# Kernel tuning notes

Measured on AMD Instinct MI355X. Metric: run time of the kernel, lower is better.

The kernel has to match this reference:

```python
import jax, jax.numpy as jnp
import numpy as np


def pairwise_dist(x):
    # Euclidean cdist via the expansion trick; grad-safe sqrt (0 grad at 0, like torch).
    sq = jnp.sum(x * x, axis=1)
    d2 = sq[:, None] + sq[None, :] - 2.0 * (x @ x.T)
    d2 = jnp.maximum(d2, 0.0)
    pos = d2 > 0
    return jnp.where(pos, jnp.sqrt(jnp.where(pos, d2, 1.0)), 0.0)


def knn_mask(dist, k):
    # per-row ascending sort; skip index 0 (self), take next k neighbors
    idx = jnp.argsort(dist, axis=1)[:, 1:k + 1]            # [N, k]
    n = dist.shape[0]
    return jnp.zeros_like(dist).at[jnp.arange(n)[:, None], idx].set(1.0)


def setup_inputs() -> dict:
    key = jax.random.key(0)
    k1, k2 = jax.random.split(key)
    N, D, K = 8192, 64, 12
    latent = jax.random.normal(k1, (N, D), dtype=jnp.float32)
    latent_norm = jnp.ones((), dtype=jnp.float32)
    X = jax.random.normal(k2, (N, D), dtype=jnp.float32)
    dist_X = pairwise_dist(X)
    pair_mask_X = knn_mask(dist_X, K)
    return {"latent": latent, "latent_norm": latent_norm,
            "dist_X": dist_X, "pair_mask_X": pair_mask_X, "k": K}


def reference(latent, latent_norm, dist_X, pair_mask_X, k):
    n = latent.shape[0]
    dist_Z = pairwise_dist(latent) / latent_norm
    pair_mask_Z = knn_mask(dist_Z, k)

    mask_diff = pair_mask_Z - pair_mask_X
    matched = (n * k - jnp.sum(mask_diff != 0) * 0.5) / (n * k)

    # match_edges == 'symmetric'
    sig1 = dist_X * pair_mask_X
    sig1_2 = dist_Z * pair_mask_X
    distance1_2 = jnp.sum(jnp.square(sig1 - sig1_2))
    sig2 = dist_Z * pair_mask_Z
    sig2_1 = dist_X * pair_mask_Z
    distance2_1 = jnp.sum(jnp.square(sig2_1 - sig2))
    distance = distance1_2 + distance2_1
    return (distance, matched, distance1_2, distance2_1)
```

## Files before the change

### kernel.cpp

```cpp
#include <hip/hip_runtime.h>
#include <stdint.h>

constexpr int NPTS = 8192;
constexpr int DIM  = 64;
constexpr int KNN  = 12;

constexpr int RT = 64;
constexpr int CT = 64;
constexpr int CS = 4;
constexpr int STRIPE = NPTS / CS;
constexpr int NCHUNK = STRIPE / CT;
constexpr int LSTR = 72;
constexpr int BSTR = 65;

constexpr int NWG_DZ = (NPTS / RT) * CS;
constexpr int TOT4   = NPTS * NPTS / 4;
constexpr int WG4    = TOT4 / NWG_DZ;
constexpr int CH4    = WG4 / NCHUNK;

constexpr unsigned long long SENTINEL = 0xFFFFFFFFFFFFFFFFull;

typedef short bf16x8 __attribute__((ext_vector_type(8)));
typedef float f32x4  __attribute__((ext_vector_type(4)));

#define WG_BARRIER() asm volatile("s_waitcnt lgkmcnt(0)\n\ts_barrier" ::: "memory")

__device__ __forceinline__ unsigned short f2bf(float x) {
  unsigned u = __float_as_uint(x);
  return (unsigned short)((u + 0x7FFFu + ((u >> 16) & 1u)) >> 16);
}
__device__ __forceinline__ float bf2f(unsigned short h) {
  return __uint_as_float(((unsigned)h) << 16);
}

__global__ __launch_bounds__(256) void prep_kernel(
    const float* __restrict__ latent, unsigned short* __restrict__ Lh,
    unsigned short* __restrict__ Ll, float* __restrict__ sq,
    int* __restrict__ ecnt, float* __restrict__ out) {
  int i = blockIdx.x * 256 + threadIdx.x;
  ecnt[i] = 0;
  if (i < 4) out[i] = 0.0f;
  const float4* p = reinterpret_cast<const float4*>(latent + (size_t)i * DIM);
  float s = 0.f;
#pragma unroll
  for (int t = 0; t < DIM / 4; ++t) {
    float4 v = p[t];
    s += v.x * v.x + v.y * v.y + v.z * v.z + v.w * v.w;
    ushort4 h, l;
    h.x = f2bf(v.x); l.x = f2bf(v.x - bf2f(h.x));
    h.y = f2bf(v.y); l.y = f2bf(v.y - bf2f(h.y));
    h.z = f2bf(v.z); l.z = f2bf(v.z - bf2f(h.z));
    h.w = f2bf(v.w); l.w = f2bf(v.w - bf2f(h.w));
    *reinterpret_cast<ushort4*>(Lh + (size_t)i * DIM + t * 4) = h;
    *reinterpret_cast<ushort4*>(Ll + (size_t)i * DIM + t * 4) = l;
  }
  sq[i] = s;
}

__device__ __forceinline__ void topk_insert(unsigned long long cand,
                                            unsigned long long pk[KNN]) {
#pragma unroll
  for (int s = KNN - 1; s >= 0; --s) {
    bool belongs = cand < pk[s];
    bool shift = (s > 0) && (cand < pk[s - 1]);
    unsigned long long nv = shift ? pk[s - 1] : cand;
    if (belongs) pk[s] = nv;
  }
}

__device__ __forceinline__ void push_edge(int pos, int* __restrict__ ecnt,
                                          int* __restrict__ ecol) {
  int i = pos >> 13, j = pos & (NPTS - 1);
  int slot = atomicAdd(&ecnt[i], 1);
  if (slot < KNN) ecol[i * KNN + slot] = j;
}

__global__ __launch_bounds__(256, 2) void main_kernel(
    const unsigned short* __restrict__ Lh, const unsigned short* __restrict__ Ll,
    const float* __restrict__ sq, unsigned long long* __restrict__ topk_ws,
    const float* __restrict__ mask_X, int* __restrict__ ecnt,
    int* __restrict__ ecol) {
  __shared__ unsigned short Bh[CT * LSTR], Bl[CT * LSTR];
  __shared__ float d2b[RT * BSTR];
  __shared__ int   colb[RT * BSTR];
  __shared__ int   cnt[RT];
  __shared__ float thr[RT];
  __shared__ float sqA[RT];
  __shared__ float sqB[CT];

  const int tid = threadIdx.x;
  const int tile = blockIdx.x / CS;
  const int split = blockIdx.x % CS;
  const int ib = tile * RT;
  const int jb0 = split * STRIPE;

  const int wid = tid >> 6;
  const int lane = tid & 63;
  const int quad = lane >> 4;
  const int l16 = lane & 15;
  const int wr = wid >> 1;
  const int wc = wid & 1;

  bf16x8 ahr[2][2], alr[2][2];
#pragma unroll
  for (int kk = 0; kk < 2; ++kk) {
    const int ko = kk * 32 + quad * 8;
#pragma unroll
    for (int rb = 0; rb < 2; ++rb) {
      const int row = ib + wr * 32 + rb * 16 + l16;
      ahr[kk][rb] = *reinterpret_cast<const bf16x8*>(Lh + (size_t)row * DIM + ko);
      alr[kk][rb] = *reinterpret_cast<const bf16x8*>(Ll + (size_t)row * DIM + ko);
    }
  }
  if (tid < RT) { sqA[tid] = sq[ib + tid]; thr[tid] = 3.4e38f; }

  const f32x4* mbase = reinterpret_cast<const f32x4*>(mask_X);
  const int wgBase4 = blockIdx.x * WG4;

  unsigned long long pk[KNN];
#pragma unroll
  for (int t = 0; t < KNN; ++t) pk[t] = SENTINEL;

  for (int ch = 0; ch < NCHUNK; ++ch) {
    const int jb = jb0 + ch * CT;
    WG_BARRIER();

#pragma unroll
    for (int it = 0; it < 2; ++it) {
      int f = it * 256 + tid;
      int r = f >> 3, c = f & 7;
      uint4 vh = *reinterpret_cast<const uint4*>(Lh + (size_t)(jb + r) * DIM + c * 8);
      uint4 vl = *reinterpret_cast<const uint4*>(Ll + (size_t)(jb + r) * DIM + c * 8);
      *reinterpret_cast<uint4*>(&Bh[r * LSTR + c * 8]) = vh;
      *reinterpret_cast<uint4*>(&Bl[r * LSTR + c * 8]) = vl;
    }
    if (tid < CT) sqB[tid] = sq[jb + tid];
    if (tid < RT) cnt[tid] = 0;

    __builtin_amdgcn_sched_barrier(0);
    f32x4 m[4];
    const int mb = wgBase4 + ch * CH4 + tid;
#pragma unroll
    for (int q = 0; q < 4; ++q)
      m[q] = __builtin_nontemporal_load(&mbase[mb + q * 256]);

    WG_BARRIER();

    f32x4 acc[2][2];
#pragma unroll
    for (int rb = 0; rb < 2; ++rb)
#pragma unroll
      for (int cb = 0; cb < 2; ++cb) acc[rb][cb] = (f32x4){0.f, 0.f, 0.f, 0.f};

#pragma unroll
    for (int kk = 0; kk < 2; ++kk) {
      const int ko = kk * 32 + quad * 8;
      bf16x8 bh[2], bl[2];
#pragma unroll
      for (int cb = 0; cb < 2; ++cb) {
        int col = wc * 32 + cb * 16 + l16;
        bh[cb] = *reinterpret_cast<const bf16x8*>(&Bh[col * LSTR + ko]);
        bl[cb] = *reinterpret_cast<const bf16x8*>(&Bl[col * LSTR + ko]);
      }
#pragma unroll
      for (int rb = 0; rb < 2; ++rb)
#pragma unroll
        for (int cb = 0; cb < 2; ++cb) {
          acc[rb][cb] = __builtin_amdgcn_mfma_f32_16x16x32_bf16(ahr[kk][rb], bh[cb], acc[rb][cb], 0, 0, 0);
          acc[rb][cb] = __builtin_amdgcn_mfma_f32_16x16x32_bf16(ahr[kk][rb], bl[cb], acc[rb][cb], 0, 0, 0);
          acc[rb][cb] = __builtin_amdgcn_mfma_f32_16x16x32_bf16(alr[kk][rb], bh[cb], acc[rb][cb], 0, 0, 0);
        }
    }

#pragma unroll
    for (int rb = 0; rb < 2; ++rb) {
      const int row0 = wr * 32 + rb * 16 + quad * 4;
#pragma unroll
      for (int r = 0; r < 4; ++r) {
        const int rl = row0 + r;
        const int gi = ib + rl;
        const float sa = sqA[rl];
        const float t_thr = thr[rl];
#pragma unroll
        for (int cb = 0; cb < 2; ++cb) {
          const int col_l = wc * 32 + cb * 16 + l16;
          const int gj = jb + col_l;
          float d2 = sa + sqB[col_l] - 2.0f * acc[rb][cb][r];
          float d2c = fmaxf(d2, 0.0f);
          if (d2c < t_thr && gj != gi) {
            int pos = atomicAdd(&cnt[rl], 1);
            d2b[rl * BSTR + pos] = d2c;
            colb[rl * BSTR + pos] = gj;
          }
        }
      }
    }
    WG_BARRIER();

    if (tid < RT) {
      int n = cnt[tid];
      for (int t = 0; t < n; ++t) {
        unsigned long long cand =
            ((unsigned long long)__float_as_uint(d2b[tid * BSTR + t]) << 32) |
            (unsigned)colb[tid * BSTR + t];
        if (cand < pk[KNN - 1]) topk_insert(cand, pk);
      }
      thr[tid] = __uint_as_float((unsigned)(pk[KNN - 1] >> 32));
    }

#pragma unroll
    for (int q = 0; q < 4; ++q) {
      f32x4 mv = m[q];
      if (mv[0] == 0.f && mv[1] == 0.f && mv[2] == 0.f && mv[3] == 0.f) continue;
      const int base = (mb + q * 256) * 4;
      if (mv[0] != 0.f) push_edge(base + 0, ecnt, ecol);
      if (mv[1] != 0.f) push_edge(base + 1, ecnt, ecol);
      if (mv[2] != 0.f) push_edge(base + 2, ecnt, ecol);
      if (mv[3] != 0.f) push_edge(base + 3, ecnt, ecol);
    }
  }

  if (tid < RT) {
    size_t base = ((size_t)(ib + tid) * CS + split) * KNN;
#pragma unroll
    for (int t = 0; t < KNN; ++t) topk_ws[base + t] = pk[t];
  }
}

__global__ __launch_bounds__(256) void tail_kernel(
    const float* __restrict__ latent, const float* __restrict__ latent_norm,
    const float* __restrict__ dist_X, const int* __restrict__ ecol,
    const unsigned long long* __restrict__ topk_ws, float* __restrict__ d_out) {
  __shared__ float red[256];
  const int tid = threadIdx.x;
  const float invnorm = 1.0f / latent_norm[0];

  if (blockIdx.x < (NPTS * KNN / 256)) {
    const int e = blockIdx.x * 256 + tid;
    int i = e / KNN;
    int j = ecol[e];
    float dx = dist_X[(size_t)i * NPTS + j];
    const float4* a = reinterpret_cast<const float4*>(latent + (size_t)i * DIM);
    const float4* b = reinterpret_cast<const float4*>(latent + (size_t)j * DIM);
    float d2 = 0.f;
#pragma unroll
    for (int t = 0; t < DIM / 4; ++t) {
      float4 va = a[t], vb = b[t];
      float ex = va.x - vb.x, ey = va.y - vb.y, ez = va.z - vb.z, ew = va.w - vb.w;
      d2 += ex * ex + ey * ey + ez * ez + ew * ew;
    }
    float dz = (d2 > 0.f) ? sqrtf(d2) * invnorm : 0.f;
    float diff = dx - dz;

    red[tid] = diff * diff;
    __syncthreads();
    for (int s = 128; s > 0; s >>= 1) {
      if (tid < s) red[tid] += red[tid + s];
      __syncthreads();
    }
    if (tid == 0) {
      atomicAdd(&d_out[2], red[0]);
      atomicAdd(&d_out[0], red[0]);
    }
  } else {
    const int gi = (blockIdx.x - NPTS * KNN / 256) * 256 + tid;

    unsigned long long pk[KNN];
#pragma unroll
    for (int t = 0; t < KNN; ++t) pk[t] = SENTINEL;

    const unsigned long long* src = topk_ws + (size_t)gi * CS * KNN;
    for (int t = 0; t < CS * KNN; ++t) {
      unsigned long long cand = src[t];
      if (cand < pk[KNN - 1]) topk_insert(cand, pk);
    }

    int ec[KNN];
#pragma unroll
    for (int t = 0; t < KNN; ++t) ec[t] = ecol[gi * KNN + t];

    float acc2 = 0.f, accc = 0.f;
#pragma unroll
    for (int t = 0; t < KNN; ++t) {
      int j = (int)(unsigned)(pk[t] & 0xFFFFFFFFull);
      float d2 = __uint_as_float((unsigned)(pk[t] >> 32));
      float dz = (d2 > 0.0f) ? sqrtf(d2) * invnorm : 0.0f;
      float dxv = dist_X[(size_t)gi * NPTS + j];
      float diff = dxv - dz;
      acc2 += diff * diff;
      int hit = 0;
#pragma unroll
      for (int s = 0; s < KNN; ++s) hit |= (ec[s] == j);
      accc += (float)hit;
    }

    red[tid] = acc2;
    __syncthreads();
    for (int s = 128; s > 0; s >>= 1) {
      if (tid < s) red[tid] += red[tid + s];
      __syncthreads();
    }
    float racc2 = red[0];
    __syncthreads();
    red[tid] = accc;
    __syncthreads();
    for (int s = 128; s > 0; s >>= 1) {
      if (tid < s) red[tid] += red[tid + s];
      __syncthreads();
    }
    if (tid == 0) {
      atomicAdd(&d_out[3], racc2);
      atomicAdd(&d_out[0], racc2);
      atomicAdd(&d_out[1], red[0] * (1.0f / ((float)NPTS * (float)KNN)));
    }
  }
}

extern "C" void kernel_launch(void* const* d_in, const int* in_sizes, int n_in,
                              void* d_out, int out_size, void* d_ws,
                              size_t ws_size, hipStream_t stream) {
  const float* latent      = (const float*)d_in[0];
  const float* latent_norm = (const float*)d_in[1];
  const float* dist_X      = (const float*)d_in[2];
  const float* mask_X      = (const float*)d_in[3];
  float* out = (float*)d_out;

  char* w = (char*)d_ws;
  float*          sq   = (float*)w;                    w += NPTS * 4;
  unsigned short* Lh   = (unsigned short*)w;           w += NPTS * DIM * 2;
  unsigned short* Ll   = (unsigned short*)w;           w += NPTS * DIM * 2;
  int*            ecnt = (int*)w;                      w += NPTS * 4;
  int*            ecol = (int*)w;                      w += NPTS * KNN * 4;
  unsigned long long* topk = (unsigned long long*)w;

  prep_kernel<<<NPTS / 256, 256, 0, stream>>>(latent, Lh, Ll, sq, ecnt, out);
  main_kernel<<<NWG_DZ, 256, 0, stream>>>(Lh, Ll, sq, topk, mask_X, ecnt, ecol);
  tail_kernel<<<NPTS * KNN / 256 + NPTS / 256, 256, 0, stream>>>(
      latent, latent_norm, dist_X, ecol, topk, out);
}
```

Baseline: 620.7 us.

## Double-buffer column tiles, shrink candidate buffers with overflow retry, raise occupancy

Column tiles are now double-buffered: the next chunk's global loads are issued before the MFMA work and written to the alternate LDS buffer, which removes one barrier per chunk and hides load latency. The per-row candidate buffer shrinks from 65 to 28 entries, and an overflow loop reprocesses any leftover candidates, so LDS use drops. With less LDS per block and twice as many column splits, the occupancy hint rises from 2 to 3 workgroups and there are more, shorter workgroups. The cost is extra retry rounds when a row overflows, which is likely in early chunks while the threshold is still loose, plus the higher register pressure that the tighter launch bound brings.

After: 707.4 us. 14.0% more time.

```diff
diff --git a/kernel.cpp b/kernel.cpp
--- a/kernel.cpp
+++ b/kernel.cpp
@@ -7,11 +7,12 @@
 
 constexpr int RT = 64;
 constexpr int CT = 64;
-constexpr int CS = 4;
+constexpr int CS = 8;
 constexpr int STRIPE = NPTS / CS;
 constexpr int NCHUNK = STRIPE / CT;
 constexpr int LSTR = 72;
-constexpr int BSTR = 65;
+constexpr int CAP  = 28;
+constexpr int BSTR = 29;
 
 constexpr int NWG_DZ = (NPTS / RT) * CS;
 constexpr int TOT4   = NPTS * NPTS / 4;
@@ -75,18 +76,19 @@
   if (slot < KNN) ecol[i * KNN + slot] = j;
 }
 
-__global__ __launch_bounds__(256, 2) void main_kernel(
+__global__ __launch_bounds__(256, 3) void main_kernel(
     const unsigned short* __restrict__ Lh, const unsigned short* __restrict__ Ll,
     const float* __restrict__ sq, unsigned long long* __restrict__ topk_ws,
     const float* __restrict__ mask_X, int* __restrict__ ecnt,
     int* __restrict__ ecol) {
-  __shared__ unsigned short Bh[CT * LSTR], Bl[CT * LSTR];
+  __shared__ unsigned short Bh[2 * CT * LSTR], Bl[2 * CT * LSTR];
   __shared__ float d2b[RT * BSTR];
   __shared__ int   colb[RT * BSTR];
   __shared__ int   cnt[RT];
   __shared__ float thr[RT];
   __shared__ float sqA[RT];
-  __shared__ float sqB[CT];
+  __shared__ float sqB[2][CT];
+  __shared__ int   ovf;
 
   const int tid = threadIdx.x;
   const int tile = blockIdx.x / CS;
@@ -112,7 +114,20 @@
       alr[kk][rb] = *reinterpret_cast<const bf16x8*>(Ll + (size_t)row * DIM + ko);
     }
   }
-  if (tid < RT) { sqA[tid] = sq[ib + tid]; thr[tid] = 3.4e38f; }
+  if (tid < RT) { sqA[tid] = sq[ib + tid]; thr[tid] = 3.4e38f; cnt[tid] = 0; }
+
+  {
+#pragma unroll
+    for (int it = 0; it < 2; ++it) {
+      int f = it * 256 + tid, r = f >> 3, c = f & 7;
+      uint4 vh = *reinterpret_cast<const uint4*>(Lh + (size_t)(jb0 + r) * DIM + c * 8);
+      uint4 vl = *reinterpret_cast<const uint4*>(Ll + (size_t)(jb0 + r) * DIM + c * 8);
+      *reinterpret_cast<uint4*>(&Bh[r * LSTR + c * 8]) = vh;
+      *reinterpret_cast<uint4*>(&Bl[r * LSTR + c * 8]) = vl;
+    }
+    if (tid < CT) sqB[0][tid] = sq[jb0 + tid];
+  }
+  __syncthreads();
 
   const f32x4* mbase = reinterpret_cast<const f32x4*>(mask_X);
   const int wgBase4 = blockIdx.x * WG4;
@@ -122,30 +137,33 @@
   for (int t = 0; t < KNN; ++t) pk[t] = SENTINEL;
 
   for (int ch = 0; ch < NCHUNK; ++ch) {
+    const int cur = ch & 1, nxt = cur ^ 1;
     const int jb = jb0 + ch * CT;
-    WG_BARRIER();
-
-#pragma unroll
-    for (int it = 0; it < 2; ++it) {
-      int f = it * 256 + tid;
-      int r = f >> 3, c = f & 7;
-      uint4 vh = *reinterpret_cast<const uint4*>(Lh + (size_t)(jb + r) * DIM + c * 8);
-      uint4 vl = *reinterpret_cast<const uint4*>(Ll + (size_t)(jb + r) * DIM + c * 8);
-      *reinterpret_cast<uint4*>(&Bh[r * LSTR + c * 8]) = vh;
-      *reinterpret_cast<uint4*>(&Bl[r * LSTR + c * 8]) = vl;
-    }
-    if (tid < CT) sqB[tid] = sq[jb + tid];
-    if (tid < RT) cnt[tid] = 0;
-
-    __builtin_amdgcn_sched_barrier(0);
+    const bool have_next = (ch + 1 < NCHUNK);
+
+    uint4 vh0, vl0, vh1, vl1;
+    float sqn = 0.f;
+    if (have_next) {
+      {
+        int f = tid, r = f >> 3, c = f & 7;
+        vh0 = *reinterpret_cast<const uint4*>(Lh + (size_t)(jb + CT + r) * DIM + c * 8);
+        vl0 = *reinterpret_cast<const uint4*>(Ll + (size_t)(jb + CT + r) * DIM + c * 8);
+      }
+      {
+        int f = 256 + tid, r = f >> 3, c = f & 7;
+        vh1 = *reinterpret_cast<const uint4*>(Lh + (size_t)(jb + CT + r) * DIM + c * 8);
+        vl1 = *reinterpret_cast<const uint4*>(Ll + (size_t)(jb + CT + r) * DIM + c * 8);
+      }
+      if (tid < CT) sqn = sq[jb + CT + tid];
+    }
     f32x4 m[4];
     const int mb = wgBase4 + ch * CH4 + tid;
 #pragma unroll
     for (int q = 0; q < 4; ++q)
       m[q] = __builtin_nontemporal_load(&mbase[mb + q * 256]);
-
-    WG_BARRIER();
-
+    __builtin_amdgcn_sched_barrier(0);
+
+    const int bbase = cur * CT * LSTR;
     f32x4 acc[2][2];
 #pragma unroll
     for (int rb = 0; rb < 2; ++rb)
@@ -159,8 +177,8 @@
 #pragma unroll
       for (int cb = 0; cb < 2; ++cb) {
         int col = wc * 32 + cb * 16 + l16;
-        bh[cb] = *reinterpret_cast<const bf16x8*>(&Bh[col * LSTR + ko]);
-        bl[cb] = *reinterpret_cast<const bf16x8*>(&Bl[col * LSTR + ko]);
+        bh[cb] = *reinterpret_cast<const bf16x8*>(&Bh[bbase + col * LSTR + ko]);
+        bl[cb] = *reinterpret_cast<const bf16x8*>(&Bl[bbase + col * LSTR + ko]);
       }
 #pragma unroll
       for (int rb = 0; rb < 2; ++rb)
@@ -172,52 +190,81 @@
         }
     }
 
-#pragma unroll
-    for (int rb = 0; rb < 2; ++rb) {
-      const int row0 = wr * 32 + rb * 16 + quad * 4;
-#pragma unroll
-      for (int r = 0; r < 4; ++r) {
-        const int rl = row0 + r;
-        const int gi = ib + rl;
-        const float sa = sqA[rl];
-        const float t_thr = thr[rl];
-#pragma unroll
-        for (int cb = 0; cb < 2; ++cb) {
-          const int col_l = wc * 32 + cb * 16 + l16;
-          const int gj = jb + col_l;
-          float d2 = sa + sqB[col_l] - 2.0f * acc[rb][cb][r];
-          float d2c = fmaxf(d2, 0.0f);
-          if (d2c < t_thr && gj != gi) {
-            int pos = atomicAdd(&cnt[rl], 1);
-            d2b[rl * BSTR + pos] = d2c;
-            colb[rl * BSTR + pos] = gj;
+    unsigned todo = 0xFFFFu;
+    int round = 0;
+    do {
+#pragma unroll
+      for (int rb = 0; rb < 2; ++rb) {
+#pragma unroll
+        for (int r = 0; r < 4; ++r) {
+          const int rl = wr * 32 + rb * 16 + quad * 4 + r;
+          const int gi = ib + rl;
+          const float sa = sqA[rl];
+          const float tt = thr[rl];
+#pragma unroll
+          for (int cb = 0; cb < 2; ++cb) {
+            const unsigned bit = 1u << (rb * 8 + r * 2 + cb);
+            if (todo & bit) {
+              const int col_l = wc * 32 + cb * 16 + l16;
+              const int gj = jb + col_l;
+              float d2 = sa + sqB[cur][col_l] - 2.0f * acc[rb][cb][r];
+              float d2c = fmaxf(d2, 0.0f);
+              if (d2c < tt && gj != gi) {
+                int pos = atomicAdd(&cnt[rl], 1);
+                if (pos < CAP) {
+                  d2b[rl * BSTR + pos] = d2c;
+                  colb[rl * BSTR + pos] = gj;
+                  todo &= ~bit;
+                }
+              } else {
+                todo &= ~bit;
+              }
+            }
           }
         }
       }
-    }
-    WG_BARRIER();
-
-    if (tid < RT) {
-      int n = cnt[tid];
-      for (int t = 0; t < n; ++t) {
-        unsigned long long cand =
-            ((unsigned long long)__float_as_uint(d2b[tid * BSTR + t]) << 32) |
-            (unsigned)colb[tid * BSTR + t];
-        if (cand < pk[KNN - 1]) topk_insert(cand, pk);
-      }
-      thr[tid] = __uint_as_float((unsigned)(pk[KNN - 1] >> 32));
-    }
-
-#pragma unroll
-    for (int q = 0; q < 4; ++q) {
-      f32x4 mv = m[q];
-      if (mv[0] == 0.f && mv[1] == 0.f && mv[2] == 0.f && mv[3] == 0.f) continue;
-      const int base = (mb + q * 256) * 4;
-      if (mv[0] != 0.f) push_edge(base + 0, ecnt, ecol);
-      if (mv[1] != 0.f) push_edge(base + 1, ecnt, ecol);
-      if (mv[2] != 0.f) push_edge(base + 2, ecnt, ecol);
-      if (mv[3] != 0.f) push_edge(base + 3, ecnt, ecol);
-    }
+      if (round == 0 && have_next) {
+        const int boff = nxt * CT * LSTR;
+        { int f = tid, r = f >> 3, c = f & 7;
+          *reinterpret_cast<uint4*>(&Bh[boff + r * LSTR + c * 8]) = vh0;
+          *reinterpret_cast<uint4*>(&Bl[boff + r * LSTR + c * 8]) = vl0; }
+        { int f = 256 + tid, r = f >> 3, c = f & 7;
+          *reinterpret_cast<uint4*>(&Bh[boff + r * LSTR + c * 8]) = vh1;
+          *reinterpret_cast<uint4*>(&Bl[boff + r * LSTR + c * 8]) = vl1; }
+        if (tid < CT) sqB[nxt][tid] = sqn;
+      }
+      WG_BARRIER();
+
+      if (tid < RT) {
+        const int nraw = cnt[tid];
+        const int n = nraw > CAP ? CAP : nraw;
+        for (int t = 0; t < n; ++t) {
+          unsigned long long cand =
+              ((unsigned long long)__float_as_uint(d2b[tid * BSTR + t]) << 32) |
+              (unsigned)colb[tid * BSTR + t];
+          if (cand < pk[KNN - 1]) topk_insert(cand, pk);
+        }
+        thr[tid] = __uint_as_float((unsigned)(pk[KNN - 1] >> 32));
+        cnt[tid] = 0;
+        bool o = nraw > CAP;
+        bool anyo = __any(o);
+        if (tid == 0) ovf = anyo ? 1 : 0;
+      }
+      if (round == 0) {
+#pragma unroll
+        for (int q = 0; q < 4; ++q) {
+          f32x4 mv = m[q];
+          if (mv[0] == 0.f && mv[1] == 0.f && mv[2] == 0.f && mv[3] == 0.f) continue;
+          const int base = (mb + q * 256) * 4;
+          if (mv[0] != 0.f) push_edge(base + 0, ecnt, ecol);
+          if (mv[1] != 0.f) push_edge(base + 1, ecnt, ecol);
+          if (mv[2] != 0.f) push_edge(base + 2, ecnt, ecol);
+          if (mv[3] != 0.f) push_edge(base + 3, ecnt, ecol);
+        }
+      }
+      WG_BARRIER();
+      ++round;
+    } while (ovf != 0);
   }
 
   if (tid < RT) {
```
